# Performance work log

Hardware: AMD Instinct MI355X
Metric: run time of the kernel (lower is better)

## Reference

```python
import jax, jax.numpy as jnp
import numpy as np


def _lin(x, w, b):
    return x @ w + b


def _fmv(x, w):
    # fused weighted mean/variance over the views axis (dim 2)
    mean = jnp.sum(x * w, axis=2, keepdims=True)
    var = jnp.sum(w * (x - mean) ** 2, axis=2, keepdims=True)
    return mean, var


def setup_inputs() -> dict:
    key = jax.random.key(0)
    ks = iter(jax.random.split(key, 40))
    R, S, V = 2048, 64, 8  # n_rays, n_samples, n_views

    def W(i, o):
        return jax.random.normal(next(ks), (i, o), jnp.float32) * (1.0 / np.sqrt(i))

    inp = {
        "rgb_feat": jax.random.normal(next(ks), (R, S, V, 35), jnp.float32),
        "neuray_feat": jax.random.normal(next(ks), (R, S, V, 32), jnp.float32),
        "ray_diff": jax.random.normal(next(ks), (R, S, V, 4), jnp.float32),
        "mask": (jax.random.uniform(next(ks), (R, S, V, 1)) > 0.1).astype(jnp.float32),
        "que_pts": jax.random.normal(next(ks), (R, S, 3), jnp.float32),
        "que_dir": jax.random.normal(next(ks), (R, S, 3), jnp.float32),
        # ray_dir_fc: Linear(4,16) ELU Linear(16,35) ELU
        "rd_w1": W(4, 16), "rd_b1": jnp.zeros(16, jnp.float32),
        "rd_w2": W(16, 35), "rd_b2": jnp.zeros(35, jnp.float32),
        # rgbfeat_fc: Linear(35,64) ReLU Linear(64,64)
        "rf_w1": W(35, 64), "rf_b1": jnp.zeros(64, jnp.float32),
        "rf_w2": W(64, 64), "rf_b2": jnp.zeros(64, jnp.float32),
        # neuray_fc: Linear(32,8) ELU Linear(8,1)
        "nr_w1": W(32, 8), "nr_b1": jnp.zeros(8, jnp.float32),
        "nr_w2": W(8, 1), "nr_b2": jnp.zeros(1, jnp.float32),
        # base_fc: Linear(207,64) ELU Linear(64,32) ELU
        "base_w1": W(207, 64), "base_b1": jnp.zeros(64, jnp.float32),
        "base_w2": W(64, 32), "base_b2": jnp.zeros(32, jnp.float32),
        # vis_fc: Linear(32,32) ELU Linear(32,33) ELU
        "vis_w1": W(32, 32), "vis_b1": jnp.zeros(32, jnp.float32),
        "vis_w2": W(32, 33), "vis_b2": jnp.zeros(33, jnp.float32),
        # vis_fc2: Linear(32,32) ELU Linear(32,1) Sigmoid
        "v2_w1": W(32, 32), "v2_b1": jnp.zeros(32, jnp.float32),
        "v2_w2": W(32, 1), "v2_b2": jnp.zeros(1, jnp.float32),
    }
    return inp


def reference(rgb_feat, neuray_feat, ray_diff, mask, que_pts, que_dir,
              rd_w1, rd_b1, rd_w2, rd_b2,
              rf_w1, rf_b1, rf_w2, rf_b2,
              nr_w1, nr_b1, nr_w2, nr_b2,
              base_w1, base_b1, base_w2, base_b2,
              vis_w1, vis_b1, vis_w2, vis_b2,
              v2_w1, v2_b1, v2_w2, v2_b2):
    elu = jax.nn.elu
    num_views = rgb_feat.shape[2]

    direction_feat = elu(_lin(elu(_lin(ray_diff, rd_w1, rd_b1)), rd_w2, rd_b2))
    rgb_feat_ = rgb_feat + direction_feat  # [R,S,V,35]

    rgb_feat_1 = _lin(jax.nn.relu(_lin(rgb_feat, rf_w1, rf_b1)), rf_w2, rf_b2)
    rgb_feat_max = jnp.max(rgb_feat_1, axis=2)  # [R,S,64]

    weight = mask / (jnp.sum(mask, axis=2, keepdims=True) + 1e-8)
    weight0 = jax.nn.sigmoid(_lin(elu(_lin(neuray_feat, nr_w1, nr_b1)), nr_w2, nr_b2))

    mean0, var0 = _fmv(rgb_feat_, weight0)
    mean1, var1 = _fmv(rgb_feat_, weight)
    globalfeat = jnp.concatenate([mean0, var0, mean1, var1], axis=-1)  # [R,S,1,140]

    gshape = globalfeat.shape[:2] + (num_views, globalfeat.shape[-1])
    x = jnp.concatenate([jnp.broadcast_to(globalfeat, gshape), rgb_feat_, neuray_feat], axis=-1)  # [R,S,V,207]
    x = elu(_lin(elu(_lin(x, base_w1, base_b1)), base_w2, base_b2))  # [R,S,V,32]

    x_vis = elu(_lin(elu(_lin(x * weight, vis_w1, vis_b1)), vis_w2, vis_b2))  # [R,S,V,33]
    x_res, vis = x_vis[..., :-1], x_vis[..., -1:]
    vis = jax.nn.sigmoid(vis) * mask
    x = x + x_res
    vis = jax.nn.sigmoid(_lin(elu(_lin(x * vis, v2_w1, v2_b1)), v2_w2, v2_b2)) * mask
    weight2 = vis / (jnp.sum(vis, axis=2, keepdims=True) + 1e-8)

    mean, var = _fmv(x, weight2)
    out = jnp.concatenate([mean[:, :, 0], var[:, :, 0]], axis=-1) + rgb_feat_max  # [R,S,64]
    return out
```

## Files before the change

### kernel.cpp

```cpp
#include <hip/hip_runtime.h>


#define NRS (2048*64)
#define T 4

__device__ __forceinline__ float eluf(float x){ return x > 0.f ? x : __expf(x)-1.f; }
__device__ __forceinline__ float sigmf(float x){ return 1.f/(1.f+__expf(-x)); }
__device__ __forceinline__ float4 elu4(float4 a){
    return make_float4(eluf(a.x), eluf(a.y), eluf(a.z), eluf(a.w));
}

#define FMA4(A, X, W) do { \
    A.x = fmaf((X).x, (W), A.x); \
    A.y = fmaf((X).y, (W), A.y); \
    A.z = fmaf((X).z, (W), A.z); \
    A.w = fmaf((X).w, (W), A.w); } while(0)

__global__ __launch_bounds__(256, 4) void nerf_fused(
    const float* __restrict__ g_rgb,  const float* __restrict__ g_nr,
    const float* __restrict__ g_rd,   const float* __restrict__ g_mask,
    const float* __restrict__ rd_w1,  const float* __restrict__ rd_b1,
    const float* __restrict__ rd_w2,  const float* __restrict__ rd_b2,
    const float* __restrict__ rf_w1,  const float* __restrict__ rf_b1,
    const float* __restrict__ rf_w2,  const float* __restrict__ rf_b2,
    const float* __restrict__ nr_w1,  const float* __restrict__ nr_b1,
    const float* __restrict__ nr_w2,  const float* __restrict__ nr_b2,
    const float* __restrict__ base_w1,const float* __restrict__ base_b1,
    const float* __restrict__ base_w2,const float* __restrict__ base_b2,
    const float* __restrict__ vis_w1, const float* __restrict__ vis_b1,
    const float* __restrict__ vis_w2, const float* __restrict__ vis_b2,
    const float* __restrict__ v2_w1,  const float* __restrict__ v2_b1,
    const float* __restrict__ v2_w2,  const float* __restrict__ v2_b2,
    float* __restrict__ out)
{
    __shared__ __align__(16) float s_rgb [8][35][T];
    __shared__ __align__(16) float s_nr  [8][32][T];
    __shared__ __align__(16) float s_rd  [8][4][T];
    __shared__ __align__(16) float s_h16 [8][16][T];
    __shared__ __align__(16) float s_h8  [8][8][T];
    __shared__ __align__(16) float s_hid [8][64][T];
    __shared__ __align__(16) float s_f1  [8][64][T];
    __shared__ __align__(16) float s_x   [8][32][T];
    __shared__ float s_gmax[T][64];
    __shared__ float s_global[T][140];
    __shared__ float s_gc  [T][64];
    __shared__ float s_mask[T][8];
    __shared__ float s_w0  [T][8];
    __shared__ float s_wt  [T][8];
    __shared__ float s_vis [T][8];

    const int rs0 = blockIdx.x * T;
    const int tid = threadIdx.x;
    const int v   = tid >> 5;
    const int l   = tid & 31;

    {
        const float* src = g_rgb + (size_t)rs0 * 280;
        for (int idx = tid; idx < 1120; idx += 256) {
            const int t = idx / 280;
            const int r = idx - t * 280;
            const int vv = r / 35;
            const int f  = r - vv * 35;
            s_rgb[vv][f][t] = src[idx];
        }
        const float* srcn = g_nr + (size_t)rs0 * 256;
        for (int idx = tid; idx < 1024; idx += 256)
            s_nr[(idx >> 5) & 7][idx & 31][idx >> 8] = srcn[idx];
        if (tid < 128)
            s_rd[(tid >> 2) & 7][tid & 3][tid >> 5] = g_rd[(size_t)rs0 * 32 + tid];
        if (tid < 32)
            s_mask[tid >> 3][tid & 7] = g_mask[(size_t)rs0 * 8 + tid];
    }
    __syncthreads();

    {
        const float b0 = rf_b1[l], b1 = rf_b1[l + 32];
        float4 a0 = make_float4(b0, b0, b0, b0);
        float4 a1 = make_float4(b1, b1, b1, b1);
        #pragma unroll
        for (int i = 0; i < 35; ++i) {
            const float4 xv = *reinterpret_cast<const float4*>(s_rgb[v][i]);
            const float w0 = rf_w1[i*64 + l];
            const float w1 = rf_w1[i*64 + l + 32];
            FMA4(a0, xv, w0);
            FMA4(a1, xv, w1);
        }
        *reinterpret_cast<float4*>(s_hid[v][l]) =
            make_float4(fmaxf(a0.x,0.f), fmaxf(a0.y,0.f), fmaxf(a0.z,0.f), fmaxf(a0.w,0.f));
        *reinterpret_cast<float4*>(s_hid[v][l+32]) =
            make_float4(fmaxf(a1.x,0.f), fmaxf(a1.y,0.f), fmaxf(a1.z,0.f), fmaxf(a1.w,0.f));

        if (l < 16) {
            const float bb = rd_b1[l];
            float4 acc = make_float4(bb, bb, bb, bb);
            #pragma unroll
            for (int i = 0; i < 4; ++i) {
                const float4 xv = *reinterpret_cast<const float4*>(s_rd[v][i]);
                FMA4(acc, xv, rd_w1[i*16 + l]);
            }
            *reinterpret_cast<float4*>(s_h16[v][l]) = elu4(acc);
        } else if (l < 24) {
            const int o = l - 16;
            const float bb = nr_b1[o];
            float4 acc = make_float4(bb, bb, bb, bb);
            #pragma unroll
            for (int i = 0; i < 32; ++i) {
                const float4 xv = *reinterpret_cast<const float4*>(s_nr[v][i]);
                FMA4(acc, xv, nr_w1[i*8 + o]);
            }
            *reinterpret_cast<float4*>(s_h8[v][o]) = elu4(acc);
        }
    }
    __syncthreads();

    {
        for (int o = l; o < 35; o += 32) {
            const float bb = rd_b2[o];
            float4 acc = make_float4(bb, bb, bb, bb);
            #pragma unroll
            for (int i = 0; i < 16; ++i) {
                const float4 h = *reinterpret_cast<const float4*>(s_h16[v][i]);
                FMA4(acc, h, rd_w2[i*35 + o]);
            }
            float4 r = *reinterpret_cast<const float4*>(s_rgb[v][o]);
            r.x += eluf(acc.x); r.y += eluf(acc.y); r.z += eluf(acc.z); r.w += eluf(acc.w);
            *reinterpret_cast<float4*>(s_rgb[v][o]) = r;
        }

        const float b0 = rf_b2[l], b1 = rf_b2[l + 32];
        float4 a0 = make_float4(b0, b0, b0, b0);
        float4 a1 = make_float4(b1, b1, b1, b1);
        #pragma unroll
        for (int i = 0; i < 64; ++i) {
            const float4 h = *reinterpret_cast<const float4*>(s_hid[v][i]);
            FMA4(a0, h, rf_w2[i*64 + l]);
            FMA4(a1, h, rf_w2[i*64 + l + 32]);
        }
        *reinterpret_cast<float4*>(s_f1[v][l])    = a0;
        *reinterpret_cast<float4*>(s_f1[v][l+32]) = a1;

        if (tid < 32) {
            const int tt = tid >> 3, vv = tid & 7;
            float acc = nr_b2[0];
            #pragma unroll
            for (int i = 0; i < 8; ++i) acc = fmaf(s_h8[vv][i][tt], nr_w2[i], acc);
            s_w0[tt][vv] = sigmf(acc);
        } else if (tid < 64) {
            const int tt = (tid - 32) >> 3, vv = tid & 7;
            float ms = 0.f;
            #pragma unroll
            for (int i = 0; i < 8; ++i) ms += s_mask[tt][i];
            s_wt[tt][vv] = s_mask[tt][vv] / (ms + 1e-8f);
        }
    }
    __syncthreads();

    {
        const int tg = tid >> 6, og = tid & 63;
        float m = s_f1[0][og][tg];
        #pragma unroll
        for (int vv = 1; vv < 8; ++vv) m = fmaxf(m, s_f1[vv][og][tg]);
        s_gmax[tg][og] = m;

        if (tid < 140) {
            const int tt = tid / 35, f = tid - tt * 35;
            float m0 = 0.f, m1 = 0.f;
            #pragma unroll
            for (int vv = 0; vv < 8; ++vv) {
                const float p = s_rgb[vv][f][tt];
                m0 = fmaf(p, s_w0[tt][vv], m0);
                m1 = fmaf(p, s_wt[tt][vv], m1);
            }
            float v0 = 0.f, v1 = 0.f;
            #pragma unroll
            for (int vv = 0; vv < 8; ++vv) {
                const float p = s_rgb[vv][f][tt];
                const float d0 = p - m0, d1 = p - m1;
                v0 = fmaf(s_w0[tt][vv] * d0, d0, v0);
                v1 = fmaf(s_wt[tt][vv] * d1, d1, v1);
            }
            s_global[tt][f]       = m0;
            s_global[tt][35 + f]  = v0;
            s_global[tt][70 + f]  = m1;
            s_global[tt][105 + f] = v1;
        }
    }
    __syncthreads();

    float4 pa0 = make_float4(0.f, 0.f, 0.f, 0.f);
    float4 pa1 = make_float4(0.f, 0.f, 0.f, 0.f);
    {
        const int tg = tid >> 6, og = tid & 63;
        float acc = 0.f;
        #pragma unroll 10
        for (int i = 0; i < 140; ++i) acc = fmaf(s_global[tg][i], base_w1[i*64 + og], acc);
        s_gc[tg][og] = acc;

        #pragma unroll
        for (int i = 0; i < 35; ++i) {
            const float4 xv = *reinterpret_cast<const float4*>(s_rgb[v][i]);
            FMA4(pa0, xv, base_w1[(140+i)*64 + l]);
            FMA4(pa1, xv, base_w1[(140+i)*64 + l + 32]);
        }
        #pragma unroll
        for (int i = 0; i < 32; ++i) {
            const float4 xv = *reinterpret_cast<const float4*>(s_nr[v][i]);
            FMA4(pa0, xv, base_w1[(175+i)*64 + l]);
            FMA4(pa1, xv, base_w1[(175+i)*64 + l + 32]);
        }
    }
    __syncthreads();

    {
        const float b0 = base_b1[l], b1 = base_b1[l + 32];
        float4 h0, h1;
        h0.x = eluf(pa0.x + s_gc[0][l] + b0);
        h0.y = eluf(pa0.y + s_gc[1][l] + b0);
        h0.z = eluf(pa0.z + s_gc[2][l] + b0);
        h0.w = eluf(pa0.w + s_gc[3][l] + b0);
        h1.x = eluf(pa1.x + s_gc[0][l+32] + b1);
        h1.y = eluf(pa1.y + s_gc[1][l+32] + b1);
        h1.z = eluf(pa1.z + s_gc[2][l+32] + b1);
        h1.w = eluf(pa1.w + s_gc[3][l+32] + b1);
        *reinterpret_cast<float4*>(s_hid[v][l])    = h0;
        *reinterpret_cast<float4*>(s_hid[v][l+32]) = h1;
    }
    __syncthreads();

    {
        const float bb = base_b2[l];
        float4 acc = make_float4(bb, bb, bb, bb);
        #pragma unroll
        for (int i = 0; i < 64; ++i) {
            const float4 h = *reinterpret_cast<const float4*>(s_hid[v][i]);
            FMA4(acc, h, base_w2[i*32 + l]);
        }
        *reinterpret_cast<float4*>(s_x[v][l]) = elu4(acc);
    }
    __syncthreads();

    {
        float4 acc = make_float4(0.f, 0.f, 0.f, 0.f);
        #pragma unroll
        for (int i = 0; i < 32; ++i) {
            const float4 x = *reinterpret_cast<const float4*>(s_x[v][i]);
            FMA4(acc, x, vis_w1[i*32 + l]);
        }
        const float bb = vis_b1[l];
        float4 h;
        h.x = eluf(acc.x * s_wt[0][v] + bb);
        h.y = eluf(acc.y * s_wt[1][v] + bb);
        h.z = eluf(acc.z * s_wt[2][v] + bb);
        h.w = eluf(acc.w * s_wt[3][v] + bb);
        *reinterpret_cast<float4*>(s_hid[v][l]) = h;
    }
    __syncthreads();

    {
        const float bb = vis_b2[l];
        float4 acc = make_float4(bb, bb, bb, bb);
        #pragma unroll
        for (int i = 0; i < 32; ++i) {
            const float4 h = *reinterpret_cast<const float4*>(s_hid[v][i]);
            FMA4(acc, h, vis_w2[i*33 + l]);
        }
        float4 x = *reinterpret_cast<const float4*>(s_x[v][l]);
        x.x += eluf(acc.x); x.y += eluf(acc.y); x.z += eluf(acc.z); x.w += eluf(acc.w);
        *reinterpret_cast<float4*>(s_x[v][l]) = x;

        if (tid < 32) {
            const int tt = tid >> 3, vv = tid & 7;
            float a2 = vis_b2[32];
            #pragma unroll
            for (int i = 0; i < 32; ++i) a2 = fmaf(s_hid[vv][i][tt], vis_w2[i*33 + 32], a2);
            s_vis[tt][vv] = sigmf(eluf(a2)) * s_mask[tt][vv];
        }
    }
    __syncthreads();

    {
        float4 acc = make_float4(0.f, 0.f, 0.f, 0.f);
        #pragma unroll
        for (int i = 0; i < 32; ++i) {
            const float4 x = *reinterpret_cast<const float4*>(s_x[v][i]);
            FMA4(acc, x, v2_w1[i*32 + l]);
        }
        const float bb = v2_b1[l];
        float4 h;
        h.x = eluf(acc.x * s_vis[0][v] + bb);
        h.y = eluf(acc.y * s_vis[1][v] + bb);
        h.z = eluf(acc.z * s_vis[2][v] + bb);
        h.w = eluf(acc.w * s_vis[3][v] + bb);
        *reinterpret_cast<float4*>(s_hid[v][l]) = h;
    }
    __syncthreads();

    if (tid < 32) {
        const int tt = tid >> 3, vv = tid & 7;
        float acc = v2_b2[0];
        #pragma unroll
        for (int i = 0; i < 32; ++i) acc = fmaf(s_hid[vv][i][tt], v2_w2[i], acc);
        s_vis[tt][vv] = sigmf(acc) * s_mask[tt][vv];
    }
    __syncthreads();

    if (tid < 128) {
        const int tt = tid >> 5, col = tid & 31;
        float vs = 0.f;
        #pragma unroll
        for (int vv = 0; vv < 8; ++vv) vs += s_vis[tt][vv];
        const float inv = 1.f / (vs + 1e-8f);
        float mean = 0.f;
        #pragma unroll
        for (int vv = 0; vv < 8; ++vv) mean = fmaf(s_x[vv][col][tt], s_vis[tt][vv], mean);
        mean *= inv;
        float var = 0.f;
        #pragma unroll
        for (int vv = 0; vv < 8; ++vv) {
            const float d = s_x[vv][col][tt] - mean;
            var = fmaf(s_vis[tt][vv] * d, d, var);
        }
        var *= inv;
        const size_t ob = ((size_t)rs0 + tt) * 64;
        out[ob + col]      = mean + s_gmax[tt][col];
        out[ob + 32 + col] = var  + s_gmax[tt][32 + col];
    }
}

extern "C" void kernel_launch(void* const* d_in, const int* in_sizes, int n_in,
                              void* d_out, int out_size, void* d_ws, size_t ws_size,
                              hipStream_t stream) {
    const float* g_rgb   = (const float*)d_in[0];
    const float* g_nr    = (const float*)d_in[1];
    const float* g_rd    = (const float*)d_in[2];
    const float* g_mask  = (const float*)d_in[3];
    const float* rd_w1   = (const float*)d_in[6];
    const float* rd_b1   = (const float*)d_in[7];
    const float* rd_w2   = (const float*)d_in[8];
    const float* rd_b2   = (const float*)d_in[9];
    const float* rf_w1   = (const float*)d_in[10];
    const float* rf_b1   = (const float*)d_in[11];
    const float* rf_w2   = (const float*)d_in[12];
    const float* rf_b2   = (const float*)d_in[13];
    const float* nr_w1   = (const float*)d_in[14];
    const float* nr_b1   = (const float*)d_in[15];
    const float* nr_w2   = (const float*)d_in[16];
    const float* nr_b2   = (const float*)d_in[17];
    const float* base_w1 = (const float*)d_in[18];
    const float* base_b1 = (const float*)d_in[19];
    const float* base_w2 = (const float*)d_in[20];
    const float* base_b2 = (const float*)d_in[21];
    const float* vis_w1  = (const float*)d_in[22];
    const float* vis_b1  = (const float*)d_in[23];
    const float* vis_w2  = (const float*)d_in[24];
    const float* vis_b2  = (const float*)d_in[25];
    const float* v2_w1   = (const float*)d_in[26];
    const float* v2_b1   = (const float*)d_in[27];
    const float* v2_w2   = (const float*)d_in[28];
    const float* v2_b2   = (const float*)d_in[29];
    float* out = (float*)d_out;

    hipLaunchKernelGGL(nerf_fused, dim3(NRS / T), dim3(256), 0, stream,
        g_rgb, g_nr, g_rd, g_mask,
        rd_w1, rd_b1, rd_w2, rd_b2,
        rf_w1, rf_b1, rf_w2, rf_b2,
        nr_w1, nr_b1, nr_w2, nr_b2,
        base_w1, base_b1, base_w2, base_b2,
        vis_w1, vis_b1, vis_w2, vis_b2,
        v2_w1, v2_b1, v2_w2, v2_b2,
        out);
}
```

Before: 1.320 ms.

## Rewrite fused kernel as one thread per (ray,sample,view) with register MLPs

Replaces the 256-thread block, which staged activations in LDS for 4 ray-samples, with a 64-lane block covering 8 ray-samples. Each lane owns one view and runs every MLP layer from registers, reading the weights as wave-uniform loads. Reductions over the view axis use xor shuffles, and the global-feature part of base_fc is computed once per sample and shared through LDS. This removes most LDS traffic and barriers, at the cost of very high register pressure (64-wide accumulators plus the input arrays) and uncoalesced strided per-thread input loads.

```diff
diff --git a/kernel.cpp b/kernel.cpp
--- a/kernel.cpp
+++ b/kernel.cpp
@@ -2,21 +2,17 @@
 
 
 #define NRS (2048*64)
-#define T 4
 
 __device__ __forceinline__ float eluf(float x){ return x > 0.f ? x : __expf(x)-1.f; }
 __device__ __forceinline__ float sigmf(float x){ return 1.f/(1.f+__expf(-x)); }
-__device__ __forceinline__ float4 elu4(float4 a){
-    return make_float4(eluf(a.x), eluf(a.y), eluf(a.z), eluf(a.w));
+__device__ __forceinline__ float sum8(float x){
+    x += __shfl_xor(x, 1); x += __shfl_xor(x, 2); x += __shfl_xor(x, 4); return x;
 }
-
-#define FMA4(A, X, W) do { \
-    A.x = fmaf((X).x, (W), A.x); \
-    A.y = fmaf((X).y, (W), A.y); \
-    A.z = fmaf((X).z, (W), A.z); \
-    A.w = fmaf((X).w, (W), A.w); } while(0)
-
-__global__ __launch_bounds__(256, 4) void nerf_fused(
+__device__ __forceinline__ float max8(float x){
+    x = fmaxf(x, __shfl_xor(x, 1)); x = fmaxf(x, __shfl_xor(x, 2)); x = fmaxf(x, __shfl_xor(x, 4)); return x;
+}
+
+__global__ __launch_bounds__(64, 2) void nerf_main(
     const float* __restrict__ g_rgb,  const float* __restrict__ g_nr,
     const float* __restrict__ g_rd,   const float* __restrict__ g_mask,
     const float* __restrict__ rd_w1,  const float* __restrict__ rd_b1,
@@ -33,298 +29,239 @@
     const float* __restrict__ v2_w2,  const float* __restrict__ v2_b2,
     float* __restrict__ out)
 {
-    __shared__ __align__(16) float s_rgb [8][35][T];
-    __shared__ __align__(16) float s_nr  [8][32][T];
-    __shared__ __align__(16) float s_rd  [8][4][T];
-    __shared__ __align__(16) float s_h16 [8][16][T];
-    __shared__ __align__(16) float s_h8  [8][8][T];
-    __shared__ __align__(16) float s_hid [8][64][T];
-    __shared__ __align__(16) float s_f1  [8][64][T];
-    __shared__ __align__(16) float s_x   [8][32][T];
-    __shared__ float s_gmax[T][64];
-    __shared__ float s_global[T][140];
-    __shared__ float s_gc  [T][64];
-    __shared__ float s_mask[T][8];
-    __shared__ float s_w0  [T][8];
-    __shared__ float s_wt  [T][8];
-    __shared__ float s_vis [T][8];
-
-    const int rs0 = blockIdx.x * T;
-    const int tid = threadIdx.x;
-    const int v   = tid >> 5;
-    const int l   = tid & 31;
-
-    {
-        const float* src = g_rgb + (size_t)rs0 * 280;
-        for (int idx = tid; idx < 1120; idx += 256) {
-            const int t = idx / 280;
-            const int r = idx - t * 280;
-            const int vv = r / 35;
-            const int f  = r - vv * 35;
-            s_rgb[vv][f][t] = src[idx];
-        }
-        const float* srcn = g_nr + (size_t)rs0 * 256;
-        for (int idx = tid; idx < 1024; idx += 256)
-            s_nr[(idx >> 5) & 7][idx & 31][idx >> 8] = srcn[idx];
-        if (tid < 128)
-            s_rd[(tid >> 2) & 7][tid & 3][tid >> 5] = g_rd[(size_t)rs0 * 32 + tid];
-        if (tid < 32)
-            s_mask[tid >> 3][tid & 7] = g_mask[(size_t)rs0 * 8 + tid];
+    __shared__ __align__(16) float g_lds[8*144];
+    __shared__ float gc_lds  [8*65];
+    __shared__ float gmax_lds[8*65];
+    __shared__ float out_lds [512];
+
+    const int lane = threadIdx.x;
+    const int t    = lane >> 3;
+    const int v    = lane & 7;
+    const int pid  = blockIdx.x * 64 + lane;
+
+    float rgb[35];
+    #pragma unroll
+    for (int k = 0; k < 35; ++k) rgb[k] = g_rgb[(size_t)pid*35 + k];
+    float rdv[4];
+    #pragma unroll
+    for (int k = 0; k < 4; ++k) rdv[k] = g_rd[(size_t)pid*4 + k];
+    float nrv[32];
+    #pragma unroll
+    for (int k = 0; k < 32; ++k) nrv[k] = g_nr[(size_t)pid*32 + k];
+    const float mask = g_mask[pid];
+    const float wt   = mask / (sum8(mask) + 1e-8f);
+
+    float x64[64];
+    {
+        float acc[64];
+        #pragma unroll
+        for (int o = 0; o < 64; ++o) acc[o] = rf_b1[o];
+        #pragma unroll 1
+        for (int k = 0; k < 35; ++k) {
+            const float xk = rgb[k];
+            #pragma unroll
+            for (int o = 0; o < 64; ++o) acc[o] = fmaf(xk, rf_w1[k*64 + o], acc[o]);
+        }
+        #pragma unroll
+        for (int o = 0; o < 64; ++o) x64[o] = fmaxf(acc[o], 0.f);
+    }
+
+    {
+        float h16[16];
+        #pragma unroll
+        for (int o = 0; o < 16; ++o) {
+            float a = rd_b1[o];
+            #pragma unroll
+            for (int k = 0; k < 4; ++k) a = fmaf(rdv[k], rd_w1[k*16 + o], a);
+            h16[o] = eluf(a);
+        }
+        #pragma unroll 1
+        for (int o = 0; o < 35; ++o) {
+            float a = rd_b2[o];
+            #pragma unroll
+            for (int k = 0; k < 16; ++k) a = fmaf(h16[k], rd_w2[k*35 + o], a);
+            rgb[o] += eluf(a);
+        }
+    }
+
+    {
+        float acc[64];
+        #pragma unroll
+        for (int o = 0; o < 64; ++o) acc[o] = rf_b2[o];
+        #pragma unroll 1
+        for (int k = 0; k < 64; ++k) {
+            const float xk = x64[k];
+            #pragma unroll
+            for (int o = 0; o < 64; ++o) acc[o] = fmaf(xk, rf_w2[k*64 + o], acc[o]);
+        }
+        #pragma unroll
+        for (int o = 0; o < 64; ++o) {
+            const float gm = max8(acc[o]);
+            if (v == (o & 7)) gmax_lds[t*65 + o] = gm;
+        }
+    }
+
+    float w0;
+    {
+        float h8[8];
+        #pragma unroll
+        for (int o = 0; o < 8; ++o) h8[o] = nr_b1[o];
+        #pragma unroll 4
+        for (int k = 0; k < 32; ++k) {
+            const float xk = nrv[k];
+            #pragma unroll
+            for (int o = 0; o < 8; ++o) h8[o] = fmaf(xk, nr_w1[k*8 + o], h8[o]);
+        }
+        float a = nr_b2[0];
+        #pragma unroll
+        for (int k = 0; k < 8; ++k) a = fmaf(eluf(h8[k]), nr_w2[k], a);
+        w0 = sigmf(a);
+    }
+
+    #pragma unroll 2
+    for (int f = 0; f < 35; ++f) {
+        const float a  = rgb[f];
+        const float m0 = sum8(w0 * a);
+        const float d0 = a - m0;
+        const float v0 = sum8(w0 * d0 * d0);
+        const float m1 = sum8(wt * a);
+        const float d1 = a - m1;
+        const float v1 = sum8(wt * d1 * d1);
+        if (v == (f & 7)) {
+            g_lds[t*144 + f]       = m0;
+            g_lds[t*144 + 35 + f]  = v0;
+            g_lds[t*144 + 70 + f]  = m1;
+            g_lds[t*144 + 105 + f] = v1;
+        }
     }
     __syncthreads();
 
     {
-        const float b0 = rf_b1[l], b1 = rf_b1[l + 32];
-        float4 a0 = make_float4(b0, b0, b0, b0);
-        float4 a1 = make_float4(b1, b1, b1, b1);
-        #pragma unroll
-        for (int i = 0; i < 35; ++i) {
-            const float4 xv = *reinterpret_cast<const float4*>(s_rgb[v][i]);
-            const float w0 = rf_w1[i*64 + l];
-            const float w1 = rf_w1[i*64 + l + 32];
-            FMA4(a0, xv, w0);
-            FMA4(a1, xv, w1);
-        }
-        *reinterpret_cast<float4*>(s_hid[v][l]) =
-            make_float4(fmaxf(a0.x,0.f), fmaxf(a0.y,0.f), fmaxf(a0.z,0.f), fmaxf(a0.w,0.f));
-        *reinterpret_cast<float4*>(s_hid[v][l+32]) =
-            make_float4(fmaxf(a1.x,0.f), fmaxf(a1.y,0.f), fmaxf(a1.z,0.f), fmaxf(a1.w,0.f));
-
-        if (l < 16) {
-            const float bb = rd_b1[l];
-            float4 acc = make_float4(bb, bb, bb, bb);
-            #pragma unroll
-            for (int i = 0; i < 4; ++i) {
-                const float4 xv = *reinterpret_cast<const float4*>(s_rd[v][i]);
-                FMA4(acc, xv, rd_w1[i*16 + l]);
+        float ga[8];
+        #pragma unroll
+        for (int q = 0; q < 8; ++q) ga[q] = 0.f;
+        #pragma unroll 1
+        for (int i = 0; i < 140; i += 4) {
+            float w_[4];
+            #pragma unroll
+            for (int j = 0; j < 4; ++j) w_[j] = base_w1[(i + j)*64 + lane];
+            #pragma unroll
+            for (int q = 0; q < 8; ++q) {
+                const float4 gv = *reinterpret_cast<const float4*>(&g_lds[q*144 + i]);
+                ga[q] = fmaf(gv.x, w_[0], ga[q]);
+                ga[q] = fmaf(gv.y, w_[1], ga[q]);
+                ga[q] = fmaf(gv.z, w_[2], ga[q]);
+                ga[q] = fmaf(gv.w, w_[3], ga[q]);
             }
-            *reinterpret_cast<float4*>(s_h16[v][l]) = elu4(acc);
-        } else if (l < 24) {
-            const int o = l - 16;
-            const float bb = nr_b1[o];
-            float4 acc = make_float4(bb, bb, bb, bb);
-            #pragma unroll
-            for (int i = 0; i < 32; ++i) {
-                const float4 xv = *reinterpret_cast<const float4*>(s_nr[v][i]);
-                FMA4(acc, xv, nr_w1[i*8 + o]);
+        }
+        #pragma unroll
+        for (int q = 0; q < 8; ++q) gc_lds[q*65 + lane] = ga[q];
+    }
+    __syncthreads();
+
+    {
+        float acc[64];
+        #pragma unroll
+        for (int o = 0; o < 64; ++o) acc[o] = base_b1[o] + gc_lds[t*65 + o];
+        #pragma unroll 1
+        for (int k = 0; k < 35; ++k) {
+            const float xk = rgb[k];
+            #pragma unroll
+            for (int o = 0; o < 64; ++o) acc[o] = fmaf(xk, base_w1[(140+k)*64 + o], acc[o]);
+        }
+        #pragma unroll 1
+        for (int k = 0; k < 32; ++k) {
+            const float xk = nrv[k];
+            #pragma unroll
+            for (int o = 0; o < 64; ++o) acc[o] = fmaf(xk, base_w1[(175+k)*64 + o], acc[o]);
+        }
+        #pragma unroll
+        for (int o = 0; o < 64; ++o) x64[o] = eluf(acc[o]);
+    }
+
+    float x2[32];
+    {
+        #pragma unroll
+        for (int o = 0; o < 32; ++o) x2[o] = base_b2[o];
+        #pragma unroll 2
+        for (int k = 0; k < 64; ++k) {
+            const float xk = x64[k];
+            #pragma unroll
+            for (int o = 0; o < 32; ++o) x2[o] = fmaf(xk, base_w2[k*32 + o], x2[o]);
+        }
+        #pragma unroll
+        for (int o = 0; o < 32; ++o) x2[o] = eluf(x2[o]);
+    }
+
+    float hv[32];
+    {
+        float acc[32];
+        #pragma unroll
+        for (int o = 0; o < 32; ++o) acc[o] = 0.f;
+        #pragma unroll 2
+        for (int k = 0; k < 32; ++k) {
+            const float xk = x2[k];
+            #pragma unroll
+            for (int o = 0; o < 32; ++o) acc[o] = fmaf(xk, vis_w1[k*32 + o], acc[o]);
+        }
+        #pragma unroll
+        for (int o = 0; o < 32; ++o) hv[o] = eluf(fmaf(acc[o], wt, vis_b1[o]));
+    }
+    float vis1;
+    {
+        float acc[32];
+        #pragma unroll
+        for (int o = 0; o < 32; ++o) acc[o] = vis_b2[o];
+        float a2 = vis_b2[32];
+        #pragma unroll 2
+        for (int k = 0; k < 32; ++k) {
+            const float hk = hv[k];
+            #pragma unroll
+            for (int o = 0; o < 32; ++o) acc[o] = fmaf(hk, vis_w2[k*33 + o], acc[o]);
+            a2 = fmaf(hk, vis_w2[k*33 + 32], a2);
+        }
+        #pragma unroll
+        for (int o = 0; o < 32; ++o) x2[o] += eluf(acc[o]);
+        vis1 = sigmf(eluf(a2)) * mask;
+    }
+
+    float vis2;
+    {
+        float acc[32];
+        #pragma unroll
+        for (int o = 0; o < 32; ++o) acc[o] = 0.f;
+        #pragma unroll 2
+        for (int k = 0; k < 32; ++k) {
+            const float xk = x2[k];
+            #pragma unroll
+            for (int o = 0; o < 32; ++o) acc[o] = fmaf(xk, v2_w1[k*32 + o], acc[o]);
+        }
+        float a = v2_b2[0];
+        #pragma unroll
+        for (int k = 0; k < 32; ++k) a = fmaf(eluf(fmaf(acc[k], vis1, v2_b1[k])), v2_w2[k], a);
+        vis2 = sigmf(a) * mask;
+    }
+
+    {
+        const float w2 = vis2 / (sum8(vis2) + 1e-8f);
+        #pragma unroll 2
+        for (int c = 0; c < 32; ++c) {
+            const float xv = x2[c];
+            const float m  = sum8(w2 * xv);
+            const float d  = xv - m;
+            const float va = sum8(w2 * d * d);
+            if (v == (c & 7)) {
+                out_lds[t*64 + c]      = m  + gmax_lds[t*65 + c];
+                out_lds[t*64 + 32 + c] = va + gmax_lds[t*65 + 32 + c];
             }
-            *reinterpret_cast<float4*>(s_h8[v][o]) = elu4(acc);
         }
     }
     __syncthreads();
 
-    {
-        for (int o = l; o < 35; o += 32) {
-            const float bb = rd_b2[o];
-            float4 acc = make_float4(bb, bb, bb, bb);
-            #pragma unroll
-            for (int i = 0; i < 16; ++i) {
-                const float4 h = *reinterpret_cast<const float4*>(s_h16[v][i]);
-                FMA4(acc, h, rd_w2[i*35 + o]);
-            }
-            float4 r = *reinterpret_cast<const float4*>(s_rgb[v][o]);
-            r.x += eluf(acc.x); r.y += eluf(acc.y); r.z += eluf(acc.z); r.w += eluf(acc.w);
-            *reinterpret_cast<float4*>(s_rgb[v][o]) = r;
-        }
-
-        const float b0 = rf_b2[l], b1 = rf_b2[l + 32];
-        float4 a0 = make_float4(b0, b0, b0, b0);
-        float4 a1 = make_float4(b1, b1, b1, b1);
-        #pragma unroll
-        for (int i = 0; i < 64; ++i) {
-            const float4 h = *reinterpret_cast<const float4*>(s_hid[v][i]);
-            FMA4(a0, h, rf_w2[i*64 + l]);
-            FMA4(a1, h, rf_w2[i*64 + l + 32]);
-        }
-        *reinterpret_cast<float4*>(s_f1[v][l])    = a0;
-        *reinterpret_cast<float4*>(s_f1[v][l+32]) = a1;
-
-        if (tid < 32) {
-            const int tt = tid >> 3, vv = tid & 7;
-            float acc = nr_b2[0];
-            #pragma unroll
-            for (int i = 0; i < 8; ++i) acc = fmaf(s_h8[vv][i][tt], nr_w2[i], acc);
-            s_w0[tt][vv] = sigmf(acc);
-        } else if (tid < 64) {
-            const int tt = (tid - 32) >> 3, vv = tid & 7;
-            float ms = 0.f;
-            #pragma unroll
-            for (int i = 0; i < 8; ++i) ms += s_mask[tt][i];
-            s_wt[tt][vv] = s_mask[tt][vv] / (ms + 1e-8f);
-        }
-    }
-    __syncthreads();
-
-    {
-        const int tg = tid >> 6, og = tid & 63;
-        float m = s_f1[0][og][tg];
-        #pragma unroll
-        for (int vv = 1; vv < 8; ++vv) m = fmaxf(m, s_f1[vv][og][tg]);
-        s_gmax[tg][og] = m;
-
-        if (tid < 140) {
-            const int tt = tid / 35, f = tid - tt * 35;
-            float m0 = 0.f, m1 = 0.f;
-            #pragma unroll
-            for (int vv = 0; vv < 8; ++vv) {
-                const float p = s_rgb[vv][f][tt];
-                m0 = fmaf(p, s_w0[tt][vv], m0);
-                m1 = fmaf(p, s_wt[tt][vv], m1);
-            }
-            float v0 = 0.f, v1 = 0.f;
-            #pragma unroll
-            for (int vv = 0; vv < 8; ++vv) {
-                const float p = s_rgb[vv][f][tt];
-                const float d0 = p - m0, d1 = p - m1;
-                v0 = fmaf(s_w0[tt][vv] * d0, d0, v0);
-                v1 = fmaf(s_wt[tt][vv] * d1, d1, v1);
-            }
-            s_global[tt][f]       = m0;
-            s_global[tt][35 + f]  = v0;
-            s_global[tt][70 + f]  = m1;
-            s_global[tt][105 + f] = v1;
-        }
-    }
-    __syncthreads();
-
-    float4 pa0 = make_float4(0.f, 0.f, 0.f, 0.f);
-    float4 pa1 = make_float4(0.f, 0.f, 0.f, 0.f);
-    {
-        const int tg = tid >> 6, og = tid & 63;
-        float acc = 0.f;
-        #pragma unroll 10
-        for (int i = 0; i < 140; ++i) acc = fmaf(s_global[tg][i], base_w1[i*64 + og], acc);
-        s_gc[tg][og] = acc;
-
-        #pragma unroll
-        for (int i = 0; i < 35; ++i) {
-            const float4 xv = *reinterpret_cast<const float4*>(s_rgb[v][i]);
-            FMA4(pa0, xv, base_w1[(140+i)*64 + l]);
-            FMA4(pa1, xv, base_w1[(140+i)*64 + l + 32]);
-        }
-        #pragma unroll
-        for (int i = 0; i < 32; ++i) {
-            const float4 xv = *reinterpret_cast<const float4*>(s_nr[v][i]);
-            FMA4(pa0, xv, base_w1[(175+i)*64 + l]);
-            FMA4(pa1, xv, base_w1[(175+i)*64 + l + 32]);
-        }
-    }
-    __syncthreads();
-
-    {
-        const float b0 = base_b1[l], b1 = base_b1[l + 32];
-        float4 h0, h1;
-        h0.x = eluf(pa0.x + s_gc[0][l] + b0);
-        h0.y = eluf(pa0.y + s_gc[1][l] + b0);
-        h0.z = eluf(pa0.z + s_gc[2][l] + b0);
-        h0.w = eluf(pa0.w + s_gc[3][l] + b0);
-        h1.x = eluf(pa1.x + s_gc[0][l+32] + b1);
-        h1.y = eluf(pa1.y + s_gc[1][l+32] + b1);
-        h1.z = eluf(pa1.z + s_gc[2][l+32] + b1);
-        h1.w = eluf(pa1.w + s_gc[3][l+32] + b1);
-        *reinterpret_cast<float4*>(s_hid[v][l])    = h0;
-        *reinterpret_cast<float4*>(s_hid[v][l+32]) = h1;
-    }
-    __syncthreads();
-
-    {
-        const float bb = base_b2[l];
-        float4 acc = make_float4(bb, bb, bb, bb);
-        #pragma unroll
-        for (int i = 0; i < 64; ++i) {
-            const float4 h = *reinterpret_cast<const float4*>(s_hid[v][i]);
-            FMA4(acc, h, base_w2[i*32 + l]);
-        }
-        *reinterpret_cast<float4*>(s_x[v][l]) = elu4(acc);
-    }
-    __syncthreads();
-
-    {
-        float4 acc = make_float4(0.f, 0.f, 0.f, 0.f);
-        #pragma unroll
-        for (int i = 0; i < 32; ++i) {
-            const float4 x = *reinterpret_cast<const float4*>(s_x[v][i]);
-            FMA4(acc, x, vis_w1[i*32 + l]);
-        }
-        const float bb = vis_b1[l];
-        float4 h;
-        h.x = eluf(acc.x * s_wt[0][v] + bb);
-        h.y = eluf(acc.y * s_wt[1][v] + bb);
-        h.z = eluf(acc.z * s_wt[2][v] + bb);
-        h.w = eluf(acc.w * s_wt[3][v] + bb);
-        *reinterpret_cast<float4*>(s_hid[v][l]) = h;
-    }
-    __syncthreads();
-
-    {
-        const float bb = vis_b2[l];
-        float4 acc = make_float4(bb, bb, bb, bb);
-        #pragma unroll
-        for (int i = 0; i < 32; ++i) {
-            const float4 h = *reinterpret_cast<const float4*>(s_hid[v][i]);
-            FMA4(acc, h, vis_w2[i*33 + l]);
-        }
-        float4 x = *reinterpret_cast<const float4*>(s_x[v][l]);
-        x.x += eluf(acc.x); x.y += eluf(acc.y); x.z += eluf(acc.z); x.w += eluf(acc.w);
-        *reinterpret_cast<float4*>(s_x[v][l]) = x;
-
-        if (tid < 32) {
-            const int tt = tid >> 3, vv = tid & 7;
-            float a2 = vis_b2[32];
-            #pragma unroll
-            for (int i = 0; i < 32; ++i) a2 = fmaf(s_hid[vv][i][tt], vis_w2[i*33 + 32], a2);
-            s_vis[tt][vv] = sigmf(eluf(a2)) * s_mask[tt][vv];
-        }
-    }
-    __syncthreads();
-
-    {
-        float4 acc = make_float4(0.f, 0.f, 0.f, 0.f);
-        #pragma unroll
-        for (int i = 0; i < 32; ++i) {
-            const float4 x = *reinterpret_cast<const float4*>(s_x[v][i]);
-            FMA4(acc, x, v2_w1[i*32 + l]);
-        }
-        const float bb = v2_b1[l];
-        float4 h;
-        h.x = eluf(acc.x * s_vis[0][v] + bb);
-        h.y = eluf(acc.y * s_vis[1][v] + bb);
-        h.z = eluf(acc.z * s_vis[2][v] + bb);
-        h.w = eluf(acc.w * s_vis[3][v] + bb);
-        *reinterpret_cast<float4*>(s_hid[v][l]) = h;
-    }
-    __syncthreads();
-
-    if (tid < 32) {
-        const int tt = tid >> 3, vv = tid & 7;
-        float acc = v2_b2[0];
-        #pragma unroll
-        for (int i = 0; i < 32; ++i) acc = fmaf(s_hid[vv][i][tt], v2_w2[i], acc);
-        s_vis[tt][vv] = sigmf(acc) * s_mask[tt][vv];
-    }
-    __syncthreads();
-
-    if (tid < 128) {
-        const int tt = tid >> 5, col = tid & 31;
-        float vs = 0.f;
-        #pragma unroll
-        for (int vv = 0; vv < 8; ++vv) vs += s_vis[tt][vv];
-        const float inv = 1.f / (vs + 1e-8f);
-        float mean = 0.f;
-        #pragma unroll
-        for (int vv = 0; vv < 8; ++vv) mean = fmaf(s_x[vv][col][tt], s_vis[tt][vv], mean);
-        mean *= inv;
-        float var = 0.f;
-        #pragma unroll
-        for (int vv = 0; vv < 8; ++vv) {
-            const float d = s_x[vv][col][tt] - mean;
-            var = fmaf(s_vis[tt][vv] * d, d, var);
-        }
-        var *= inv;
-        const size_t ob = ((size_t)rs0 + tt) * 64;
-        out[ob + col]      = mean + s_gmax[tt][col];
-        out[ob + 32 + col] = var  + s_gmax[tt][32 + col];
-    }
+    const size_t ob = (size_t)blockIdx.x * 512;
+    #pragma unroll
+    for (int j = 0; j < 8; ++j)
+        out[ob + j*64 + lane] = out_lds[j*64 + lane];
 }
 
 extern "C" void kernel_launch(void* const* d_in, const int* in_sizes, int n_in,
@@ -360,7 +297,7 @@
     const float* v2_b2   = (const float*)d_in[29];
     float* out = (float*)d_out;
 
-    hipLaunchKernelGGL(nerf_fused, dim3(NRS / T), dim3(256), 0, stream,
+    hipLaunchKernelGGL(nerf_main, dim3(NRS / 8), dim3(64), 0, stream,
         g_rgb, g_nr, g_rd, g_mask,
         rd_w1, rd_b1, rd_w2, rd_b2,
         rf_w1, rf_b1, rf_w2, rf_b2,
```

Measured after the change: 1.305 ms. About the same (-1.2%).
